# Optimization experiments

Hardware: AMD Instinct MI355X
Metric: run time of the kernel (lower is better)

## Reference

```python
import jax, jax.numpy as jnp
import numpy as np

N_IN = 8192
C_IN, C_H, C_OUT = 64, 32, 32
L = 3
GRID = 64  # parent grid extent (parents live on even coords of a 128^3 grid)


def _build_coords_and_maps():
    """Build sparse voxel coords and the 27-offset kernel map for 3x3x3 stride-1 convs."""
    rng = np.random.RandomState(0)
    pts = rng.randint(0, GRID, size=(4 * N_IN, 3))
    uniq = np.unique(pts, axis=0)
    parents = uniq[rng.permutation(uniq.shape[0])[:N_IN]] * 2  # stride-2 coords in [0,128)
    offs = np.array([[i, j, k] for i in (0, 1) for j in (0, 1) for k in (0, 1)])
    # generative conv transpose kernel=2 stride=2: child k of parent i sits at row i*8+k
    coords = (parents[:, None, :] + offs[None]).reshape(-1, 3)
    n_out = coords.shape[0]
    D = 2 * GRID
    grid = -np.ones((D, D, D), dtype=np.int64)
    grid[coords[:, 0], coords[:, 1], coords[:, 2]] = np.arange(n_out)
    k_offs = np.array([[i, j, k] for i in (-1, 0, 1) for j in (-1, 0, 1) for k in (-1, 0, 1)])
    ins, outs = [], []
    for d in k_offs:
        sh = coords + d
        valid = np.all((sh >= 0) & (sh < D), axis=1)
        j = -np.ones(n_out, dtype=np.int64)
        j[valid] = grid[sh[valid, 0], sh[valid, 1], sh[valid, 2]]
        m = j >= 0
        ins.append(j[m])
        outs.append(np.nonzero(m)[0])
    P = max(len(a) for a in ins)
    nbr_in = np.full((27, P), n_out, dtype=np.int32)   # pad -> dummy zero row
    nbr_out = np.full((27, P), n_out, dtype=np.int32)  # pad -> dummy dropped row
    for k in range(27):
        nbr_in[k, : len(ins[k])] = ins[k]
        nbr_out[k, : len(outs[k])] = outs[k]
    return jnp.asarray(nbr_in), jnp.asarray(nbr_out), n_out


def setup_inputs() -> dict:
    nbr_in, nbr_out, n_out = _build_coords_and_maps()
    key = jax.random.key(0)
    ks = jax.random.split(key, 20)
    w = lambda k, shape, fan: jax.random.normal(k, shape, jnp.float32) / np.float32(np.sqrt(fan))
    C4, C2 = C_OUT // 4, C_OUT // 2
    inp = {
        "x": jax.random.normal(ks[0], (N_IN, C_IN), jnp.float32),
        "W_up": w(ks[1], (8, C_IN, C_H), C_IN),
        "b_up": 0.01 * jax.random.normal(ks[2], (C_H,), jnp.float32),
        "W_conv": w(ks[3], (27, C_H, C_OUT), 27 * C_H),
        "b_conv": 0.01 * jax.random.normal(ks[4], (C_OUT,), jnp.float32),
        "Wb00": w(ks[5], (L, 27, C_OUT, C4), 27 * C_OUT),
        "bb00": 0.01 * jax.random.normal(ks[6], (L, C4), jnp.float32),
        "Wb01": w(ks[7], (L, 27, C4, C2), 27 * C4),
        "bb01": 0.01 * jax.random.normal(ks[8], (L, C2), jnp.float32),
        "Wb10": w(ks[9], (L, C_OUT, C4), C_OUT),
        "bb10": 0.01 * jax.random.normal(ks[10], (L, C4), jnp.float32),
        "Wb11": w(ks[11], (L, 27, C4, C4), 27 * C4),
        "bb11": 0.01 * jax.random.normal(ks[12], (L, C4), jnp.float32),
        "Wb12": w(ks[13], (L, C4, C2), C4),
        "bb12": 0.01 * jax.random.normal(ks[14], (L, C2), jnp.float32),
        "W_cls": w(ks[15], (27, C_OUT, 1), 27 * C_OUT),
        "b_cls": 0.01 * jax.random.normal(ks[16], (1,), jnp.float32),
        "nbr_in": nbr_in,
        "nbr_out": nbr_out,
        # ground-truth occupancy of out coords in target_label (precomputed set membership)
        "target": jax.random.bernoulli(ks[17], 0.5, (n_out,)),
    }
    return inp


def reference(x, W_up, b_up, W_conv, b_conv, Wb00, bb00, Wb01, bb01,
              Wb10, bb10, Wb11, bb11, Wb12, bb12, W_cls, b_cls,
              nbr_in, nbr_out, target):
    n_out = target.shape[0]
    r = jax.nn.relu

    def sconv(f, W, b):
        # 3x3x3 stride-1 sparse conv via shared kernel map: gather -> per-offset GEMM -> scatter-add
        fpad = jnp.concatenate([f, jnp.zeros((1, f.shape[1]), f.dtype)], axis=0)
        g = fpad[nbr_in]                                   # [27, P, Cin]
        contrib = jnp.einsum('kpc,kcd->kpd', g, W)         # [27, P, Cout]
        out = jnp.zeros((n_out + 1, W.shape[2]), f.dtype)
        out = out.at[nbr_out.reshape(-1)].add(contrib.reshape(-1, W.shape[2]))
        return out[:n_out] + b

    # generative transpose kernel=2 stride=2: child k of parent i -> row i*8+k
    up = (jnp.einsum('nc,kcd->nkd', x, W_up) + b_up).reshape(n_out, -1)
    out = r(sconv(r(up), W_conv, b_conv))
    for l in range(L):  # InceptionResNet blocks (PCGCv2-style)
        p0 = sconv(r(sconv(out, Wb00[l], bb00[l])), Wb01[l], bb01[l])
        p1 = r(out @ Wb10[l] + bb10[l])
        p1 = r(sconv(p1, Wb11[l], bb11[l]))
        p1 = p1 @ Wb12[l] + bb12[l]
        out = jnp.concatenate([p0, p1], axis=-1) + out
    out_cls = sconv(out, W_cls, b_cls)                     # [n_out, 1]
    score = out_cls[:, 0]
    keep = score > 0
    # topk(.,1) fallback when everything is negative
    fallback = keep | (jnp.arange(n_out) == jnp.argmax(score))
    keep = jnp.where(jnp.max(score) < 0, fallback, keep)
    # MinkowskiPruning with static shapes: zero-mask pruned rows
    out_pruned = out * keep[:, None].astype(out.dtype)
    return out_pruned, out_cls, target, keep
```

## Files before the change

### kernel.cpp

```cpp
#include <hip/hip_runtime.h>
#include <math.h>

static inline int cdiv(long long a, int b){ return (int)((a + b - 1) / b); }
#define DEVINL __device__ __forceinline__

DEVINL float4 relu4(const float* a){
  return make_float4(fmaxf(a[0],0.f), fmaxf(a[1],0.f), fmaxf(a[2],0.f), fmaxf(a[3],0.f));
}

DEVINL void load32(float* fv, const float* __restrict__ p){
#pragma unroll
  for (int q = 0; q < 8; ++q){
    float4 v = ((const float4*)p)[q];
    fv[4*q]=v.x; fv[4*q+1]=v.y; fv[4*q+2]=v.z; fv[4*q+3]=v.w;
  }
}
DEVINL void load8(float* fv, const float* __restrict__ p){
#pragma unroll
  for (int q = 0; q < 2; ++q){
    float4 v = ((const float4*)p)[q];
    fv[4*q]=v.x; fv[4*q+1]=v.y; fv[4*q+2]=v.z; fv[4*q+3]=v.w;
  }
}

DEVINL int sib_k(int o, int op){
  return 13 + 9*(((op>>2)&1) - ((o>>2)&1))
            + 3*(((op>>1)&1) - ((o>>1)&1))
            +   ((op&1) - (o&1));
}

__global__ void k_rinit(int* __restrict__ cnt, int n){
  int i = blockIdx.x*blockDim.x + threadIdx.x;
  if (i < n) cnt[i] = 0;
}

__global__ void k_rbuild(const int* __restrict__ nin, const int* __restrict__ nout,
                         int* __restrict__ cnt, int* __restrict__ rem, int P, int N){
  int p = blockIdx.x*blockDim.x + threadIdx.x;
  if (p >= 27*P) return;
  int oi = nout[p];
  if (oi >= N) return;
  int j = nin[p];
  if ((oi >> 3) == (j >> 3)) return;
  int k = p / P;
  int pos = atomicAdd(&cnt[oi], 1);
  rem[(size_t)oi*20 + pos] = (j << 5) | k;
}

__global__ __launch_bounds__(256) void k_up(const float* __restrict__ x,
    const float* __restrict__ Wup, const float* __restrict__ bup,
    float* __restrict__ f, int Nn){
  __shared__ float Ws[64*32];
  const int kk = blockIdx.y;
  for (int e = threadIdx.x*4; e < 2048; e += 1024)
    *(float4*)&Ws[e] = *(const float4*)&Wup[(size_t)kk*2048 + e];
  __syncthreads();
  int t = threadIdx.x, cg = t & 7, nr = t >> 3;
  int n = blockIdx.x*32 + nr, c0 = cg*4;
  float4 b4 = *(const float4*)(bup + c0);
  float acc[4] = {b4.x, b4.y, b4.z, b4.w};
  float xr[64];
  const float4* xp = (const float4*)(x + (size_t)n*64);
#pragma unroll
  for (int q = 0; q < 16; ++q){
    float4 v = xp[q];
    xr[4*q]=v.x; xr[4*q+1]=v.y; xr[4*q+2]=v.z; xr[4*q+3]=v.w;
  }
#pragma unroll
  for (int cc = 0; cc < 64; ++cc){
    float4 w = *(const float4*)(Ws + cc*32 + c0);
    acc[0]=fmaf(xr[cc],w.x,acc[0]); acc[1]=fmaf(xr[cc],w.y,acc[1]);
    acc[2]=fmaf(xr[cc],w.z,acc[2]); acc[3]=fmaf(xr[cc],w.w,acc[3]);
  }
  *(float4*)(f + ((size_t)n*8 + kk)*32 + c0) = relu4(acc);
}

__global__ __launch_bounds__(512) void k_conv1(const float* __restrict__ fin,
    const float* __restrict__ Wg, const float* __restrict__ bg,
    const int* __restrict__ cnt, const int* __restrict__ rem,
    float* __restrict__ fout, int N){
  __shared__ float Ws[27*32*8];
  const int cb = blockIdx.y*8;
  int t = threadIdx.x;
  for (int m = t; m < 1728; m += 512){
    int k = m >> 6, r = m & 63, cc = r >> 1, q = r & 1;
    *(float4*)&Ws[k*256 + cc*8 + q*4] =
      *(const float4*)&Wg[((size_t)(k*32 + cc))*32 + cb + q*4];
  }
  __syncthreads();
  int o = t >> 6, lane = t & 63, p = lane >> 1, cg = lane & 1;
  int base = blockIdx.x*256 + p*8;
  int row = base + o, c0 = cg*4;
  float4 b4 = *(const float4*)(bg + cb + c0);
  float acc[4] = {b4.x,b4.y,b4.z,b4.w};
  float fv[32];
#pragma unroll
  for (int op = 0; op < 8; ++op){
    int kk = sib_k(o, op);
    load32(fv, fin + (size_t)(base+op)*32);
    const float* wk = Ws + kk*256 + c0;
#pragma unroll
    for (int cc = 0; cc < 32; ++cc){
      float4 w = *(const float4*)(wk + cc*8);
      acc[0]=fmaf(fv[cc],w.x,acc[0]); acc[1]=fmaf(fv[cc],w.y,acc[1]);
      acc[2]=fmaf(fv[cc],w.z,acc[2]); acc[3]=fmaf(fv[cc],w.w,acc[3]);
    }
  }
  int nrm = cnt[row];
  for (int s = 0; s < nrm; ++s){
    int e = rem[(size_t)row*20 + s];
    int kk = e & 31, j = e >> 5;
    load32(fv, fin + (size_t)j*32);
    const float* wk = Ws + kk*256 + c0;
#pragma unroll
    for (int cc = 0; cc < 32; ++cc){
      float4 w = *(const float4*)(wk + cc*8);
      acc[0]=fmaf(fv[cc],w.x,acc[0]); acc[1]=fmaf(fv[cc],w.y,acc[1]);
      acc[2]=fmaf(fv[cc],w.z,acc[2]); acc[3]=fmaf(fv[cc],w.w,acc[3]);
    }
  }
  *(float4*)(fout + (size_t)row*32 + cb + c0) = relu4(acc);
}

__global__ __launch_bounds__(512) void k_blk_a(const float* __restrict__ fO,
    const float* __restrict__ W00, const float* __restrict__ b00,
    const float* __restrict__ W10, const float* __restrict__ b10,
    const int* __restrict__ cnt, const int* __restrict__ rem,
    float* __restrict__ a8, float* __restrict__ b8, int N){
  __shared__ float Ws[27*256 + 256];
  int t = threadIdx.x;
  for (int m = t; m < 1728; m += 512){
    int k = m >> 6, r = m & 63, cc = r >> 1, q = r & 1;
    *(float4*)&Ws[k*256 + cc*8 + q*4] = ((const float4*)W00)[m];
  }
  if (t < 64) *(float4*)&Ws[6912 + t*4] = ((const float4*)W10)[t];
  __syncthreads();
  int o = t >> 6, lane = t & 63, p = lane >> 1, cg = lane & 1;
  int base = blockIdx.x*256 + p*8;
  int row = base + o, c0 = cg*4;
  float4 b4 = *(const float4*)(b00 + c0);
  float acc[4] = {b4.x,b4.y,b4.z,b4.w};
  float fv[32];
#pragma unroll
  for (int op = 0; op < 8; ++op){
    int kk = sib_k(o, op);
    load32(fv, fO + (size_t)(base+op)*32);
    const float* wk = Ws + kk*256 + c0;
#pragma unroll
    for (int cc = 0; cc < 32; ++cc){
      float4 w = *(const float4*)(wk + cc*8);
      acc[0]=fmaf(fv[cc],w.x,acc[0]); acc[1]=fmaf(fv[cc],w.y,acc[1]);
      acc[2]=fmaf(fv[cc],w.z,acc[2]); acc[3]=fmaf(fv[cc],w.w,acc[3]);
    }
  }
  int nrm = cnt[row];
  for (int s = 0; s < nrm; ++s){
    int e = rem[(size_t)row*20 + s];
    int kk = e & 31, j = e >> 5;
    load32(fv, fO + (size_t)j*32);
    const float* wk = Ws + kk*256 + c0;
#pragma unroll
    for (int cc = 0; cc < 32; ++cc){
      float4 w = *(const float4*)(wk + cc*8);
      acc[0]=fmaf(fv[cc],w.x,acc[0]); acc[1]=fmaf(fv[cc],w.y,acc[1]);
      acc[2]=fmaf(fv[cc],w.z,acc[2]); acc[3]=fmaf(fv[cc],w.w,acc[3]);
    }
  }
  *(float4*)(a8 + (size_t)row*8 + c0) = relu4(acc);
  load32(fv, fO + (size_t)row*32);
  float4 d4 = *(const float4*)(b10 + c0);
  float accb[4] = {d4.x,d4.y,d4.z,d4.w};
#pragma unroll
  for (int cc = 0; cc < 32; ++cc){
    float4 w = *(const float4*)(Ws + 6912 + cc*8 + c0);
    accb[0]=fmaf(fv[cc],w.x,accb[0]); accb[1]=fmaf(fv[cc],w.y,accb[1]);
    accb[2]=fmaf(fv[cc],w.z,accb[2]); accb[3]=fmaf(fv[cc],w.w,accb[3]);
  }
  *(float4*)(b8 + (size_t)row*8 + c0) = relu4(accb);
}

__global__ __launch_bounds__(512) void k_blk_b(const float* __restrict__ a8,
    const float* __restrict__ b8,
    const float* __restrict__ W01, const float* __restrict__ b01,
    const float* __restrict__ W11, const float* __restrict__ b11,
    const float* __restrict__ W12, const float* __restrict__ b12,
    const int* __restrict__ cnt, const int* __restrict__ rem,
    float* __restrict__ fout, int N){
  __shared__ float Ws[27*128 + 27*64 + 128];
  int t = threadIdx.x;
  for (int m = t; m < 864; m += 512)
    ((float4*)Ws)[m] = ((const float4*)W01)[m];
  for (int m = t; m < 432; m += 512)
    ((float4*)(Ws + 3456))[m] = ((const float4*)W11)[m];
  if (t < 32) *(float4*)&Ws[5184 + t*4] = ((const float4*)W12)[t];
  __syncthreads();
  int o = t >> 6, lane = t & 63, p = lane >> 2, cg = lane & 3;
  int base = blockIdx.x*128 + p*8;
  int row = base + o, c0 = cg*4;
  float4 b4 = *(const float4*)(b01 + c0);
  float acc0[4] = {b4.x,b4.y,b4.z,b4.w};
  float t8[8];
#pragma unroll
  for (int c = 0; c < 8; ++c) t8[c] = b11[c];
  float av[8], bv[8];
#pragma unroll
  for (int op = 0; op < 8; ++op){
    int kk = sib_k(o, op);
    load8(av, a8 + (size_t)(base+op)*8);
    load8(bv, b8 + (size_t)(base+op)*8);
    const float* w01k = Ws + kk*128 + c0;
    const float* w11k = Ws + 3456 + kk*64;
#pragma unroll
    for (int cc = 0; cc < 8; ++cc){
      float4 w = *(const float4*)(w01k + cc*16);
      acc0[0]=fmaf(av[cc],w.x,acc0[0]); acc0[1]=fmaf(av[cc],w.y,acc0[1]);
      acc0[2]=fmaf(av[cc],w.z,acc0[2]); acc0[3]=fmaf(av[cc],w.w,acc0[3]);
      float4 u0 = *(const float4*)(w11k + cc*8);
      float4 u1 = *(const float4*)(w11k + cc*8 + 4);
      t8[0]=fmaf(bv[cc],u0.x,t8[0]); t8[1]=fmaf(bv[cc],u0.y,t8[1]);
      t8[2]=fmaf(bv[cc],u0.z,t8[2]); t8[3]=fmaf(bv[cc],u0.w,t8[3]);
      t8[4]=fmaf(bv[cc],u1.x,t8[4]); t8[5]=fmaf(bv[cc],u1.y,t8[5]);
      t8[6]=fmaf(bv[cc],u1.z,t8[6]); t8[7]=fmaf(bv[cc],u1.w,t8[7]);
    }
  }
  int nrm = cnt[row];
  for (int s = 0; s < nrm; ++s){
    int e = rem[(size_t)row*20 + s];
    int kk = e & 31, j = e >> 5;
    load8(av, a8 + (size_t)j*8);
    load8(bv, b8 + (size_t)j*8);
    const float* w01k = Ws + kk*128 + c0;
    const float* w11k = Ws + 3456 + kk*64;
#pragma unroll
    for (int cc = 0; cc < 8; ++cc){
      float4 w = *(const float4*)(w01k + cc*16);
      acc0[0]=fmaf(av[cc],w.x,acc0[0]); acc0[1]=fmaf(av[cc],w.y,acc0[1]);
      acc0[2]=fmaf(av[cc],w.z,acc0[2]); acc0[3]=fmaf(av[cc],w.w,acc0[3]);
      float4 u0 = *(const float4*)(w11k + cc*8);
      float4 u1 = *(const float4*)(w11k + cc*8 + 4);
      t8[0]=fmaf(bv[cc],u0.x,t8[0]); t8[1]=fmaf(bv[cc],u0.y,t8[1]);
      t8[2]=fmaf(bv[cc],u0.z,t8[2]); t8[3]=fmaf(bv[cc],u0.w,t8[3]);
      t8[4]=fmaf(bv[cc],u1.x,t8[4]); t8[5]=fmaf(bv[cc],u1.y,t8[5]);
      t8[6]=fmaf(bv[cc],u1.z,t8[6]); t8[7]=fmaf(bv[cc],u1.w,t8[7]);
    }
  }
#pragma unroll
  for (int c = 0; c < 8; ++c) t8[c] = fmaxf(t8[c], 0.f);
  float4 d4 = *(const float4*)(b12 + c0);
  float acc1[4] = {d4.x,d4.y,d4.z,d4.w};
#pragma unroll
  for (int cc = 0; cc < 8; ++cc){
    float4 w = *(const float4*)(Ws + 5184 + cc*16 + c0);
    acc1[0]=fmaf(t8[cc],w.x,acc1[0]); acc1[1]=fmaf(t8[cc],w.y,acc1[1]);
    acc1[2]=fmaf(t8[cc],w.z,acc1[2]); acc1[3]=fmaf(t8[cc],w.w,acc1[3]);
  }
  float4* o0 = (float4*)(fout + (size_t)row*32 + c0);
  float4* o1 = (float4*)(fout + (size_t)row*32 + 16 + c0);
  float4 v0 = *o0, v1 = *o1;
  v0.x+=acc0[0]; v0.y+=acc0[1]; v0.z+=acc0[2]; v0.w+=acc0[3];
  v1.x+=acc1[0]; v1.y+=acc1[1]; v1.z+=acc1[2]; v1.w+=acc1[3];
  *o0 = v0; *o1 = v1;
}

__global__ __launch_bounds__(256) void k_cls(const float* __restrict__ fO,
    const float* __restrict__ Wc, const float* __restrict__ bc,
    const int* __restrict__ cnt, const int* __restrict__ rem,
    float* __restrict__ cls, int N){
  __shared__ float Ws[27*32];
  int t = threadIdx.x;
  if (t < 216) ((float4*)Ws)[t] = ((const float4*)Wc)[t];
  __syncthreads();
  int o = blockIdx.y*4 + (t >> 6), p = t & 63;
  int base = (blockIdx.x*64 + p)*8;
  int row = base + o;
  float acc = 0.f;
  float fv[32];
#pragma unroll
  for (int op = 0; op < 8; ++op){
    int kk = sib_k(o, op);
    load32(fv, fO + (size_t)(base+op)*32);
    const float* wk = Ws + kk*32;
#pragma unroll
    for (int c4 = 0; c4 < 8; ++c4){
      float4 w = *(const float4*)(wk + c4*4);
      acc = fmaf(fv[4*c4],w.x,acc);   acc = fmaf(fv[4*c4+1],w.y,acc);
      acc = fmaf(fv[4*c4+2],w.z,acc); acc = fmaf(fv[4*c4+3],w.w,acc);
    }
  }
  int nrm = cnt[row];
  for (int s = 0; s < nrm; ++s){
    int e = rem[(size_t)row*20 + s];
    int kk = e & 31, j = e >> 5;
    load32(fv, fO + (size_t)j*32);
    const float* wk = Ws + kk*32;
#pragma unroll
    for (int c4 = 0; c4 < 8; ++c4){
      float4 w = *(const float4*)(wk + c4*4);
      acc = fmaf(fv[4*c4],w.x,acc);   acc = fmaf(fv[4*c4+1],w.y,acc);
      acc = fmaf(fv[4*c4+2],w.z,acc); acc = fmaf(fv[4*c4+3],w.w,acc);
    }
  }
  cls[row] = acc + bc[0];
}

__global__ void k_reduce1(const float* __restrict__ s, float* __restrict__ pmax,
                          int* __restrict__ pidx, int n){
  __shared__ float sm[256]; __shared__ int si[256];
  int t = threadIdx.x;
  float v = -INFINITY; int vi = 0x7fffffff;
  for (int j = blockIdx.x*256 + t; j < n; j += gridDim.x*256){
    float w = s[j];
    if (w > v){ v = w; vi = j; }
  }
  sm[t] = v; si[t] = vi; __syncthreads();
  for (int o = 128; o > 0; o >>= 1){
    if (t < o){
      if (sm[t+o] > sm[t] || (sm[t+o] == sm[t] && si[t+o] < si[t])){ sm[t]=sm[t+o]; si[t]=si[t+o]; }
    }
    __syncthreads();
  }
  if (t == 0){ pmax[blockIdx.x] = sm[0]; pidx[blockIdx.x] = si[0]; }
}

__global__ void k_reduce2(const float* __restrict__ pmax, const int* __restrict__ pidx,
                          float* __restrict__ g, int nb){
  __shared__ float sm[256]; __shared__ int si[256];
  int t = threadIdx.x;
  sm[t] = (t < nb) ? pmax[t] : -INFINITY;
  si[t] = (t < nb) ? pidx[t] : 0x7fffffff;
  __syncthreads();
  for (int o = 128; o > 0; o >>= 1){
    if (t < o){
      if (sm[t+o] > sm[t] || (sm[t+o] == sm[t] && si[t+o] < si[t])){ sm[t]=sm[t+o]; si[t]=si[t+o]; }
    }
    __syncthreads();
  }
  if (t == 0){ g[0] = sm[0]; ((int*)g)[1] = si[0]; }
}

__global__ void k_final(const float* __restrict__ out, const float* __restrict__ cls,
                        const int* __restrict__ target, const float* __restrict__ g,
                        float* __restrict__ dout, int n_out){
  int idx = blockIdx.x*blockDim.x + threadIdx.x;
  if (idx >= n_out*32) return;
  int row = idx >> 5, c = idx & 31;
  float s = cls[row];
  bool keep = s > 0.f;
  if (g[0] < 0.f) keep = keep || (row == ((const int*)g)[1]);
  float km = keep ? 1.f : 0.f;
  dout[idx] = out[idx] * km;
  if (c == 0){
    dout[(size_t)n_out*32 + row] = s;
    dout[(size_t)n_out*33 + row] = (target[row] != 0) ? 1.f : 0.f;
    dout[(size_t)n_out*34 + row] = km;
  }
}

extern "C" void kernel_launch(void* const* d_in, const int* in_sizes, int n_in,
                              void* d_out, int out_size, void* d_ws, size_t ws_size,
                              hipStream_t stream){
  const float* x      = (const float*)d_in[0];
  const float* W_up   = (const float*)d_in[1];
  const float* b_up   = (const float*)d_in[2];
  const float* W_conv = (const float*)d_in[3];
  const float* b_conv = (const float*)d_in[4];
  const float* Wb00   = (const float*)d_in[5];
  const float* bb00   = (const float*)d_in[6];
  const float* Wb01   = (const float*)d_in[7];
  const float* bb01   = (const float*)d_in[8];
  const float* Wb10   = (const float*)d_in[9];
  const float* bb10   = (const float*)d_in[10];
  const float* Wb11   = (const float*)d_in[11];
  const float* bb11   = (const float*)d_in[12];
  const float* Wb12   = (const float*)d_in[13];
  const float* bb12   = (const float*)d_in[14];
  const float* W_cls  = (const float*)d_in[15];
  const float* b_cls  = (const float*)d_in[16];
  const int*   nbr_in = (const int*)d_in[17];
  const int*   nbr_out= (const int*)d_in[18];
  const int*   target = (const int*)d_in[19];

  const int N = in_sizes[19];
  const int P = in_sizes[17] / 27;
  const int pairsT = 27 * P;
  const int Nn = N / 8;

  int*   cnt  = (int*)d_ws;
  int*   rem  = cnt + N;
  float* wsf  = (float*)(rem + (size_t)N*20);
  float* f_tmp = wsf;
  float* f_out = f_tmp + (size_t)N*32;
  float* a8    = f_out + (size_t)N*32;
  float* b8    = a8 + (size_t)N*8;
  float* cls   = b8 + (size_t)N*8;
  float* pmax  = cls + N;
  int*   pidx  = (int*)(pmax + 256);
  float* gm    = pmax + 512;

  const int B = 256;

  k_rinit<<<cdiv(N,B),B,0,stream>>>(cnt, N);
  k_rbuild<<<cdiv((long long)pairsT,B),B,0,stream>>>(nbr_in, nbr_out, cnt, rem, P, N);

  k_up<<<dim3(Nn/32,8),B,0,stream>>>(x, W_up, b_up, f_tmp, Nn);

  k_conv1<<<dim3(N/256,4),512,0,stream>>>(f_tmp, W_conv, b_conv, cnt, rem, f_out, N);

  for (int l = 0; l < 3; ++l){
    k_blk_a<<<N/256,512,0,stream>>>(f_out, Wb00 + (size_t)l*6912, bb00 + l*8,
                                    Wb10 + (size_t)l*256, bb10 + l*8, cnt, rem, a8, b8, N);
    k_blk_b<<<N/128,512,0,stream>>>(a8, b8,
                                    Wb01 + (size_t)l*3456, bb01 + l*16,
                                    Wb11 + (size_t)l*1728, bb11 + l*8,
                                    Wb12 + (size_t)l*128, bb12 + l*16,
                                    cnt, rem, f_out, N);
  }

  k_cls<<<dim3(N/512,2),B,0,stream>>>(f_out, W_cls, b_cls, cnt, rem, cls, N);

  k_reduce1<<<256,256,0,stream>>>(cls, pmax, pidx, N);
  k_reduce2<<<1,256,0,stream>>>(pmax, pidx, gm, 256);

  k_final<<<cdiv((long long)N*32,B),B,0,stream>>>(f_out, cls, target, gm, (float*)d_out, N);
}
```

Measured before the change: 217.7 us.

## Register-block multiple parents per thread in sparse conv kernels to reuse weights

Restructures k_conv1, k_blk_a and k_blk_b so each thread accumulates outputs for several parent voxels (4 or 2) at once. Each shared-memory weight load is then reused across several rows. Channel tiles are widened (16 output channels per block in conv1) and the grid and block shapes are changed to match. The costs are more registers per thread, lower occupancy from bigger weight tiles, and serialized per-row handling of the remaining neighbours.

```diff
diff --git a/kernel.cpp b/kernel.cpp
--- a/kernel.cpp
+++ b/kernel.cpp
@@ -6,21 +6,6 @@
 
 DEVINL float4 relu4(const float* a){
   return make_float4(fmaxf(a[0],0.f), fmaxf(a[1],0.f), fmaxf(a[2],0.f), fmaxf(a[3],0.f));
-}
-
-DEVINL void load32(float* fv, const float* __restrict__ p){
-#pragma unroll
-  for (int q = 0; q < 8; ++q){
-    float4 v = ((const float4*)p)[q];
-    fv[4*q]=v.x; fv[4*q+1]=v.y; fv[4*q+2]=v.z; fv[4*q+3]=v.w;
-  }
-}
-DEVINL void load8(float* fv, const float* __restrict__ p){
-#pragma unroll
-  for (int q = 0; q < 2; ++q){
-    float4 v = ((const float4*)p)[q];
-    fv[4*q]=v.x; fv[4*q+1]=v.y; fv[4*q+2]=v.z; fv[4*q+3]=v.w;
-  }
 }
 
 DEVINL int sib_k(int o, int op){
@@ -79,104 +64,153 @@
     const float* __restrict__ Wg, const float* __restrict__ bg,
     const int* __restrict__ cnt, const int* __restrict__ rem,
     float* __restrict__ fout, int N){
-  __shared__ float Ws[27*32*8];
-  const int cb = blockIdx.y*8;
-  int t = threadIdx.x;
-  for (int m = t; m < 1728; m += 512){
-    int k = m >> 6, r = m & 63, cc = r >> 1, q = r & 1;
-    *(float4*)&Ws[k*256 + cc*8 + q*4] =
-      *(const float4*)&Wg[((size_t)(k*32 + cc))*32 + cb + q*4];
-  }
-  __syncthreads();
-  int o = t >> 6, lane = t & 63, p = lane >> 1, cg = lane & 1;
-  int base = blockIdx.x*256 + p*8;
-  int row = base + o, c0 = cg*4;
-  float4 b4 = *(const float4*)(bg + cb + c0);
-  float acc[4] = {b4.x,b4.y,b4.z,b4.w};
-  float fv[32];
-#pragma unroll
+  __shared__ float Ws[27*512];
+  const int y = blockIdx.y;
+  int t = threadIdx.x;
+  for (int m = t; m < 3456; m += 512){
+    int kk = m >> 7, r = m & 127, cc = r >> 2, c4 = r & 3;
+    *(float4*)&Ws[kk*512 + cc*16 + c4*4] =
+      *(const float4*)&Wg[((size_t)(kk*32+cc))*32 + y*16 + c4*4];
+  }
+  __syncthreads();
+  int o = t >> 6, lane = t & 63;
+  int q = lane >> 2, cg = lane & 3;
+  int pbase = blockIdx.x*64 + q*4;
+  int c0 = cg*4;
+  float4 b4 = *(const float4*)(bg + y*16 + c0);
+  float acc[4][4];
+#pragma unroll
+  for (int i = 0; i < 4; ++i){ acc[i][0]=b4.x; acc[i][1]=b4.y; acc[i][2]=b4.z; acc[i][3]=b4.w; }
+#pragma unroll 1
   for (int op = 0; op < 8; ++op){
     int kk = sib_k(o, op);
-    load32(fv, fin + (size_t)(base+op)*32);
-    const float* wk = Ws + kk*256 + c0;
-#pragma unroll
-    for (int cc = 0; cc < 32; ++cc){
-      float4 w = *(const float4*)(wk + cc*8);
-      acc[0]=fmaf(fv[cc],w.x,acc[0]); acc[1]=fmaf(fv[cc],w.y,acc[1]);
-      acc[2]=fmaf(fv[cc],w.z,acc[2]); acc[3]=fmaf(fv[cc],w.w,acc[3]);
-    }
-  }
-  int nrm = cnt[row];
-  for (int s = 0; s < nrm; ++s){
-    int e = rem[(size_t)row*20 + s];
-    int kk = e & 31, j = e >> 5;
-    load32(fv, fin + (size_t)j*32);
-    const float* wk = Ws + kk*256 + c0;
-#pragma unroll
-    for (int cc = 0; cc < 32; ++cc){
-      float4 w = *(const float4*)(wk + cc*8);
-      acc[0]=fmaf(fv[cc],w.x,acc[0]); acc[1]=fmaf(fv[cc],w.y,acc[1]);
-      acc[2]=fmaf(fv[cc],w.z,acc[2]); acc[3]=fmaf(fv[cc],w.w,acc[3]);
-    }
-  }
-  *(float4*)(fout + (size_t)row*32 + cb + c0) = relu4(acc);
-}
-
-__global__ __launch_bounds__(512) void k_blk_a(const float* __restrict__ fO,
+    const float* wk = Ws + kk*512 + c0;
+    const float* r0 = fin + ((size_t)((pbase+0)*8 + op))*32;
+    const float* r1 = fin + ((size_t)((pbase+1)*8 + op))*32;
+    const float* r2 = fin + ((size_t)((pbase+2)*8 + op))*32;
+    const float* r3 = fin + ((size_t)((pbase+3)*8 + op))*32;
+#pragma unroll
+    for (int h = 0; h < 2; ++h){
+      float fv[4][16];
+#pragma unroll
+      for (int qq = 0; qq < 4; ++qq){
+        float4 v0 = ((const float4*)r0)[h*4+qq];
+        float4 v1 = ((const float4*)r1)[h*4+qq];
+        float4 v2 = ((const float4*)r2)[h*4+qq];
+        float4 v3 = ((const float4*)r3)[h*4+qq];
+        fv[0][4*qq]=v0.x; fv[0][4*qq+1]=v0.y; fv[0][4*qq+2]=v0.z; fv[0][4*qq+3]=v0.w;
+        fv[1][4*qq]=v1.x; fv[1][4*qq+1]=v1.y; fv[1][4*qq+2]=v1.z; fv[1][4*qq+3]=v1.w;
+        fv[2][4*qq]=v2.x; fv[2][4*qq+1]=v2.y; fv[2][4*qq+2]=v2.z; fv[2][4*qq+3]=v2.w;
+        fv[3][4*qq]=v3.x; fv[3][4*qq+1]=v3.y; fv[3][4*qq+2]=v3.z; fv[3][4*qq+3]=v3.w;
+      }
+#pragma unroll
+      for (int cc = 0; cc < 16; ++cc){
+        float4 w = *(const float4*)(wk + (h*16+cc)*16);
+#pragma unroll
+        for (int i = 0; i < 4; ++i){
+          acc[i][0]=fmaf(fv[i][cc],w.x,acc[i][0]);
+          acc[i][1]=fmaf(fv[i][cc],w.y,acc[i][1]);
+          acc[i][2]=fmaf(fv[i][cc],w.z,acc[i][2]);
+          acc[i][3]=fmaf(fv[i][cc],w.w,acc[i][3]);
+        }
+      }
+    }
+  }
+#pragma unroll 1
+  for (int i = 0; i < 4; ++i){
+    int row = (pbase+i)*8 + o;
+    int nrm = cnt[row];
+    for (int s = 0; s < nrm; ++s){
+      int e = rem[(size_t)row*20 + s];
+      int kk = e & 31, jr = e >> 5;
+      const float* fr = fin + (size_t)jr*32;
+      const float* wk = Ws + kk*512 + c0;
+#pragma unroll
+      for (int cc = 0; cc < 32; ++cc){
+        float4 w = *(const float4*)(wk + cc*16);
+        float fx = fr[cc];
+        acc[i][0]=fmaf(fx,w.x,acc[i][0]); acc[i][1]=fmaf(fx,w.y,acc[i][1]);
+        acc[i][2]=fmaf(fx,w.z,acc[i][2]); acc[i][3]=fmaf(fx,w.w,acc[i][3]);
+      }
+    }
+    *(float4*)(fout + (size_t)row*32 + y*16 + c0) = relu4(acc[i]);
+  }
+}
+
+__global__ __launch_bounds__(256) void k_blk_a(const float* __restrict__ fO,
     const float* __restrict__ W00, const float* __restrict__ b00,
     const float* __restrict__ W10, const float* __restrict__ b10,
     const int* __restrict__ cnt, const int* __restrict__ rem,
     float* __restrict__ a8, float* __restrict__ b8, int N){
   __shared__ float Ws[27*256 + 256];
   int t = threadIdx.x;
-  for (int m = t; m < 1728; m += 512){
-    int k = m >> 6, r = m & 63, cc = r >> 1, q = r & 1;
-    *(float4*)&Ws[k*256 + cc*8 + q*4] = ((const float4*)W00)[m];
-  }
+  for (int m = t; m < 1728; m += 256)
+    ((float4*)Ws)[m] = ((const float4*)W00)[m];
   if (t < 64) *(float4*)&Ws[6912 + t*4] = ((const float4*)W10)[t];
   __syncthreads();
-  int o = t >> 6, lane = t & 63, p = lane >> 1, cg = lane & 1;
-  int base = blockIdx.x*256 + p*8;
-  int row = base + o, c0 = cg*4;
+  int w = t >> 6, lane = t & 63;
+  int o = 2*w + (lane >> 5);
+  int h = lane & 31, pp = h >> 1, cg = h & 1;
+  int pbase = blockIdx.x*32 + pp*2;
+  int c0 = cg*4;
   float4 b4 = *(const float4*)(b00 + c0);
-  float acc[4] = {b4.x,b4.y,b4.z,b4.w};
-  float fv[32];
-#pragma unroll
+  float acc[2][4];
+#pragma unroll
+  for (int i = 0; i < 2; ++i){ acc[i][0]=b4.x; acc[i][1]=b4.y; acc[i][2]=b4.z; acc[i][3]=b4.w; }
+#pragma unroll 1
   for (int op = 0; op < 8; ++op){
     int kk = sib_k(o, op);
-    load32(fv, fO + (size_t)(base+op)*32);
     const float* wk = Ws + kk*256 + c0;
+    float fv[2][32];
+#pragma unroll
+    for (int i = 0; i < 2; ++i){
+      const float4* p = (const float4*)(fO + ((size_t)((pbase+i)*8 + op))*32);
+#pragma unroll
+      for (int qq = 0; qq < 8; ++qq){
+        float4 v = p[qq];
+        fv[i][4*qq]=v.x; fv[i][4*qq+1]=v.y; fv[i][4*qq+2]=v.z; fv[i][4*qq+3]=v.w;
+      }
+    }
 #pragma unroll
     for (int cc = 0; cc < 32; ++cc){
-      float4 w = *(const float4*)(wk + cc*8);
-      acc[0]=fmaf(fv[cc],w.x,acc[0]); acc[1]=fmaf(fv[cc],w.y,acc[1]);
-      acc[2]=fmaf(fv[cc],w.z,acc[2]); acc[3]=fmaf(fv[cc],w.w,acc[3]);
-    }
-  }
-  int nrm = cnt[row];
-  for (int s = 0; s < nrm; ++s){
-    int e = rem[(size_t)row*20 + s];
-    int kk = e & 31, j = e >> 5;
-    load32(fv, fO + (size_t)j*32);
-    const float* wk = Ws + kk*256 + c0;
+      float4 wv = *(const float4*)(wk + cc*8);
+#pragma unroll
+      for (int i = 0; i < 2; ++i){
+        acc[i][0]=fmaf(fv[i][cc],wv.x,acc[i][0]); acc[i][1]=fmaf(fv[i][cc],wv.y,acc[i][1]);
+        acc[i][2]=fmaf(fv[i][cc],wv.z,acc[i][2]); acc[i][3]=fmaf(fv[i][cc],wv.w,acc[i][3]);
+      }
+    }
+  }
+#pragma unroll 1
+  for (int i = 0; i < 2; ++i){
+    int row = (pbase+i)*8 + o;
+    int nrm = cnt[row];
+    for (int s = 0; s < nrm; ++s){
+      int e = rem[(size_t)row*20 + s];
+      int kk = e & 31, jr = e >> 5;
+      const float* fr = fO + (size_t)jr*32;
+      const float* wk = Ws + kk*256 + c0;
+#pragma unroll
+      for (int cc = 0; cc < 32; ++cc){
+        float4 wv = *(const float4*)(wk + cc*8);
+        float fx = fr[cc];
+        acc[i][0]=fmaf(fx,wv.x,acc[i][0]); acc[i][1]=fmaf(fx,wv.y,acc[i][1]);
+        acc[i][2]=fmaf(fx,wv.z,acc[i][2]); acc[i][3]=fmaf(fx,wv.w,acc[i][3]);
+      }
+    }
+    *(float4*)(a8 + (size_t)row*8 + c0) = relu4(acc[i]);
+    const float* fr = fO + (size_t)row*32;
+    float4 d4 = *(const float4*)(b10 + c0);
+    float accb[4] = {d4.x,d4.y,d4.z,d4.w};
 #pragma unroll
     for (int cc = 0; cc < 32; ++cc){
-      float4 w = *(const float4*)(wk + cc*8);
-      acc[0]=fmaf(fv[cc],w.x,acc[0]); acc[1]=fmaf(fv[cc],w.y,acc[1]);
-      acc[2]=fmaf(fv[cc],w.z,acc[2]); acc[3]=fmaf(fv[cc],w.w,acc[3]);
-    }
-  }
-  *(float4*)(a8 + (size_t)row*8 + c0) = relu4(acc);
-  load32(fv, fO + (size_t)row*32);
-  float4 d4 = *(const float4*)(b10 + c0);
-  float accb[4] = {d4.x,d4.y,d4.z,d4.w};
-#pragma unroll
-  for (int cc = 0; cc < 32; ++cc){
-    float4 w = *(const float4*)(Ws + 6912 + cc*8 + c0);
-    accb[0]=fmaf(fv[cc],w.x,accb[0]); accb[1]=fmaf(fv[cc],w.y,accb[1]);
-    accb[2]=fmaf(fv[cc],w.z,accb[2]); accb[3]=fmaf(fv[cc],w.w,accb[3]);
-  }
-  *(float4*)(b8 + (size_t)row*8 + c0) = relu4(accb);
+      float4 wv = *(const float4*)(Ws + 6912 + cc*8 + c0);
+      float fx = fr[cc];
+      accb[0]=fmaf(fx,wv.x,accb[0]); accb[1]=fmaf(fx,wv.y,accb[1]);
+      accb[2]=fmaf(fx,wv.z,accb[2]); accb[3]=fmaf(fx,wv.w,accb[3]);
+    }
+    *(float4*)(b8 + (size_t)row*8 + c0) = relu4(accb);
+  }
 }
 
 __global__ __launch_bounds__(512) void k_blk_b(const float* __restrict__ a8,
@@ -194,72 +228,93 @@
     ((float4*)(Ws + 3456))[m] = ((const float4*)W11)[m];
   if (t < 32) *(float4*)&Ws[5184 + t*4] = ((const float4*)W12)[t];
   __syncthreads();
-  int o = t >> 6, lane = t & 63, p = lane >> 2, cg = lane & 3;
-  int base = blockIdx.x*128 + p*8;
-  int row = base + o, c0 = cg*4;
+  int o = t >> 6, lane = t & 63;
+  int q = lane >> 2, cg = lane & 3;
+  int pbase = blockIdx.x*32 + q*2;
+  int c0 = cg*4;
   float4 b4 = *(const float4*)(b01 + c0);
-  float acc0[4] = {b4.x,b4.y,b4.z,b4.w};
-  float t8[8];
-#pragma unroll
-  for (int c = 0; c < 8; ++c) t8[c] = b11[c];
-  float av[8], bv[8];
-#pragma unroll
+  float acc0[2][4];
+  float t8[2][8];
+#pragma unroll
+  for (int i = 0; i < 2; ++i){
+    acc0[i][0]=b4.x; acc0[i][1]=b4.y; acc0[i][2]=b4.z; acc0[i][3]=b4.w;
+#pragma unroll
+    for (int c = 0; c < 8; ++c) t8[i][c] = b11[c];
+  }
+#pragma unroll 1
   for (int op = 0; op < 8; ++op){
     int kk = sib_k(o, op);
-    load8(av, a8 + (size_t)(base+op)*8);
-    load8(bv, b8 + (size_t)(base+op)*8);
     const float* w01k = Ws + kk*128 + c0;
     const float* w11k = Ws + 3456 + kk*64;
+    float av[2][8], bv[2][8];
+#pragma unroll
+    for (int i = 0; i < 2; ++i){
+      const float4* pa = (const float4*)(a8 + ((size_t)((pbase+i)*8 + op))*8);
+      const float4* pb = (const float4*)(b8 + ((size_t)((pbase+i)*8 + op))*8);
+      float4 va0 = pa[0], va1 = pa[1], vb0 = pb[0], vb1 = pb[1];
+      av[i][0]=va0.x; av[i][1]=va0.y; av[i][2]=va0.z; av[i][3]=va0.w;
+      av[i][4]=va1.x; av[i][5]=va1.y; av[i][6]=va1.z; av[i][7]=va1.w;
+      bv[i][0]=vb0.x; bv[i][1]=vb0.y; bv[i][2]=vb0.z; bv[i][3]=vb0.w;
+      bv[i][4]=vb1.x; bv[i][5]=vb1.y; bv[i][6]=vb1.z; bv[i][7]=vb1.w;
+    }
 #pragma unroll
     for (int cc = 0; cc < 8; ++cc){
       float4 w = *(const float4*)(w01k + cc*16);
-      acc0[0]=fmaf(av[cc],w.x,acc0[0]); acc0[1]=fmaf(av[cc],w.y,acc0[1]);
-      acc0[2]=fmaf(av[cc],w.z,acc0[2]); acc0[3]=fmaf(av[cc],w.w,acc0[3]);
       float4 u0 = *(const float4*)(w11k + cc*8);
       float4 u1 = *(const float4*)(w11k + cc*8 + 4);
-      t8[0]=fmaf(bv[cc],u0.x,t8[0]); t8[1]=fmaf(bv[cc],u0.y,t8[1]);
-      t8[2]=fmaf(bv[cc],u0.z,t8[2]); t8[3]=fmaf(bv[cc],u0.w,t8[3]);
-      t8[4]=fmaf(bv[cc],u1.x,t8[4]); t8[5]=fmaf(bv[cc],u1.y,t8[5]);
-      t8[6]=fmaf(bv[cc],u1.z,t8[6]); t8[7]=fmaf(bv[cc],u1.w,t8[7]);
-    }
-  }
-  int nrm = cnt[row];
-  for (int s = 0; s < nrm; ++s){
-    int e = rem[(size_t)row*20 + s];
-    int kk = e & 31, j = e >> 5;
-    load8(av, a8 + (size_t)j*8);
-    load8(bv, b8 + (size_t)j*8);
-    const float* w01k = Ws + kk*128 + c0;
-    const float* w11k = Ws + 3456 + kk*64;
+#pragma unroll
+      for (int i = 0; i < 2; ++i){
+        acc0[i][0]=fmaf(av[i][cc],w.x,acc0[i][0]); acc0[i][1]=fmaf(av[i][cc],w.y,acc0[i][1]);
+        acc0[i][2]=fmaf(av[i][cc],w.z,acc0[i][2]); acc0[i][3]=fmaf(av[i][cc],w.w,acc0[i][3]);
+        t8[i][0]=fmaf(bv[i][cc],u0.x,t8[i][0]); t8[i][1]=fmaf(bv[i][cc],u0.y,t8[i][1]);
+        t8[i][2]=fmaf(bv[i][cc],u0.z,t8[i][2]); t8[i][3]=fmaf(bv[i][cc],u0.w,t8[i][3]);
+        t8[i][4]=fmaf(bv[i][cc],u1.x,t8[i][4]); t8[i][5]=fmaf(bv[i][cc],u1.y,t8[i][5]);
+        t8[i][6]=fmaf(bv[i][cc],u1.z,t8[i][6]); t8[i][7]=fmaf(bv[i][cc],u1.w,t8[i][7]);
+      }
+    }
+  }
+#pragma unroll 1
+  for (int i = 0; i < 2; ++i){
+    int row = (pbase+i)*8 + o;
+    int nrm = cnt[row];
+    for (int s = 0; s < nrm; ++s){
+      int e = rem[(size_t)row*20 + s];
+      int kk = e & 31, jr = e >> 5;
+      const float* fra = a8 + (size_t)jr*8;
+      const float* frb = b8 + (size_t)jr*8;
+      const float* wg0 = Ws + kk*128 + c0;
+      const float* wg1 = Ws + 3456 + kk*64;
+#pragma unroll
+      for (int cc = 0; cc < 8; ++cc){
+        float fa = fra[cc], fb = frb[cc];
+        float4 w = *(const float4*)(wg0 + cc*16);
+        float4 u0 = *(const float4*)(wg1 + cc*8);
+        float4 u1 = *(const float4*)(wg1 + cc*8 + 4);
+        acc0[i][0]=fmaf(fa,w.x,acc0[i][0]); acc0[i][1]=fmaf(fa,w.y,acc0[i][1]);
+        acc0[i][2]=fmaf(fa,w.z,acc0[i][2]); acc0[i][3]=fmaf(fa,w.w,acc0[i][3]);
+        t8[i][0]=fmaf(fb,u0.x,t8[i][0]); t8[i][1]=fmaf(fb,u0.y,t8[i][1]);
+        t8[i][2]=fmaf(fb,u0.z,t8[i][2]); t8[i][3]=fmaf(fb,u0.w,t8[i][3]);
+        t8[i][4]=fmaf(fb,u1.x,t8[i][4]); t8[i][5]=fmaf(fb,u1.y,t8[i][5]);
+        t8[i][6]=fmaf(fb,u1.z,t8[i][6]); t8[i][7]=fmaf(fb,u1.w,t8[i][7]);
+      }
+    }
+#pragma unroll
+    for (int c = 0; c < 8; ++c) t8[i][c] = fmaxf(t8[i][c], 0.f);
+    float4 d4 = *(const float4*)(b12 + c0);
+    float p1[4] = {d4.x,d4.y,d4.z,d4.w};
 #pragma unroll
     for (int cc = 0; cc < 8; ++cc){
-      float4 w = *(const float4*)(w01k + cc*16);
-      acc0[0]=fmaf(av[cc],w.x,acc0[0]); acc0[1]=fmaf(av[cc],w.y,acc0[1]);
-      acc0[2]=fmaf(av[cc],w.z,acc0[2]); acc0[3]=fmaf(av[cc],w.w,acc0[3]);
-      float4 u0 = *(const float4*)(w11k + cc*8);
-      float4 u1 = *(const float4*)(w11k + cc*8 + 4);
-      t8[0]=fmaf(bv[cc],u0.x,t8[0]); t8[1]=fmaf(bv[cc],u0.y,t8[1]);
-      t8[2]=fmaf(bv[cc],u0.z,t8[2]); t8[3]=fmaf(bv[cc],u0.w,t8[3]);
-      t8[4]=fmaf(bv[cc],u1.x,t8[4]); t8[5]=fmaf(bv[cc],u1.y,t8[5]);
-      t8[6]=fmaf(bv[cc],u1.z,t8[6]); t8[7]=fmaf(bv[cc],u1.w,t8[7]);
-    }
-  }
-#pragma unroll
-  for (int c = 0; c < 8; ++c) t8[c] = fmaxf(t8[c], 0.f);
-  float4 d4 = *(const float4*)(b12 + c0);
-  float acc1[4] = {d4.x,d4.y,d4.z,d4.w};
-#pragma unroll
-  for (int cc = 0; cc < 8; ++cc){
-    float4 w = *(const float4*)(Ws + 5184 + cc*16 + c0);
-    acc1[0]=fmaf(t8[cc],w.x,acc1[0]); acc1[1]=fmaf(t8[cc],w.y,acc1[1]);
-    acc1[2]=fmaf(t8[cc],w.z,acc1[2]); acc1[3]=fmaf(t8[cc],w.w,acc1[3]);
-  }
-  float4* o0 = (float4*)(fout + (size_t)row*32 + c0);
-  float4* o1 = (float4*)(fout + (size_t)row*32 + 16 + c0);
-  float4 v0 = *o0, v1 = *o1;
-  v0.x+=acc0[0]; v0.y+=acc0[1]; v0.z+=acc0[2]; v0.w+=acc0[3];
-  v1.x+=acc1[0]; v1.y+=acc1[1]; v1.z+=acc1[2]; v1.w+=acc1[3];
-  *o0 = v0; *o1 = v1;
+      float4 w = *(const float4*)(Ws + 5184 + cc*16 + c0);
+      p1[0]=fmaf(t8[i][cc],w.x,p1[0]); p1[1]=fmaf(t8[i][cc],w.y,p1[1]);
+      p1[2]=fmaf(t8[i][cc],w.z,p1[2]); p1[3]=fmaf(t8[i][cc],w.w,p1[3]);
+    }
+    float4* o0 = (float4*)(fout + (size_t)row*32 + c0);
+    float4* o1 = (float4*)(fout + (size_t)row*32 + 16 + c0);
+    float4 v0 = *o0, v1 = *o1;
+    v0.x+=acc0[i][0]; v0.y+=acc0[i][1]; v0.z+=acc0[i][2]; v0.w+=acc0[i][3];
+    v1.x+=p1[0]; v1.y+=p1[1]; v1.z+=p1[2]; v1.w+=p1[3];
+    *o0 = v0; *o1 = v1;
+  }
 }
 
 __global__ __launch_bounds__(256) void k_cls(const float* __restrict__ fO,
@@ -278,7 +333,12 @@
 #pragma unroll
   for (int op = 0; op < 8; ++op){
     int kk = sib_k(o, op);
-    load32(fv, fO + (size_t)(base+op)*32);
+    const float4* pp = (const float4*)(fO + (size_t)(base+op)*32);
+#pragma unroll
+    for (int qq = 0; qq < 8; ++qq){
+      float4 v = pp[qq];
+      fv[4*qq]=v.x; fv[4*qq+1]=v.y; fv[4*qq+2]=v.z; fv[4*qq+3]=v.w;
+    }
     const float* wk = Ws + kk*32;
 #pragma unroll
     for (int c4 = 0; c4 < 8; ++c4){
@@ -291,7 +351,12 @@
   for (int s = 0; s < nrm; ++s){
     int e = rem[(size_t)row*20 + s];
     int kk = e & 31, j = e >> 5;
-    load32(fv, fO + (size_t)j*32);
+    const float4* pp = (const float4*)(fO + (size_t)j*32);
+#pragma unroll
+    for (int qq = 0; qq < 8; ++qq){
+      float4 v = pp[qq];
+      fv[4*qq]=v.x; fv[4*qq+1]=v.y; fv[4*qq+2]=v.z; fv[4*qq+3]=v.w;
+    }
     const float* wk = Ws + kk*32;
 #pragma unroll
     for (int c4 = 0; c4 < 8; ++c4){
@@ -404,12 +469,12 @@
 
   k_up<<<dim3(Nn/32,8),B,0,stream>>>(x, W_up, b_up, f_tmp, Nn);
 
-  k_conv1<<<dim3(N/256,4),512,0,stream>>>(f_tmp, W_conv, b_conv, cnt, rem, f_out, N);
+  k_conv1<<<dim3(N/512,2),512,0,stream>>>(f_tmp, W_conv, b_conv, cnt, rem, f_out, N);
 
   for (int l = 0; l < 3; ++l){
-    k_blk_a<<<N/256,512,0,stream>>>(f_out, Wb00 + (size_t)l*6912, bb00 + l*8,
+    k_blk_a<<<Nn/32,256,0,stream>>>(f_out, Wb00 + (size_t)l*6912, bb00 + l*8,
                                     Wb10 + (size_t)l*256, bb10 + l*8, cnt, rem, a8, b8, N);
-    k_blk_b<<<N/128,512,0,stream>>>(a8, b8,
+    k_blk_b<<<Nn/32,512,0,stream>>>(a8, b8,
                                     Wb01 + (size_t)l*3456, bb01 + l*16,
                                     Wb11 + (size_t)l*1728, bb11 + l*8,
                                     Wb12 + (size_t)l*128, bb12 + l*16,
```

Result: slower. 666.7 us (+206.2%).

## Register-tile k_up and k_conv1 over four rows to reuse weight loads

Applied to the files above, without the earlier changes.

k_up now loads all eight child weight slices into shared memory once per block, and each thread computes four rows by four channels. k_conv1 moves from 8-channel to 16-channel output slices and also gives each thread four parent rows, so every shared-memory weight read feeds four rows of FMAs. The aim is to cut LDS traffic and redundant weight staging. The cost is more registers per thread, larger shared allocations (64 KB and 54 KB) that may lower occupancy, and fewer blocks in k_conv1.

```diff
diff --git a/kernel.cpp b/kernel.cpp
--- a/kernel.cpp
+++ b/kernel.cpp
@@ -47,79 +47,122 @@
   rem[(size_t)oi*20 + pos] = (j << 5) | k;
 }
 
-__global__ __launch_bounds__(256) void k_up(const float* __restrict__ x,
+__global__ __launch_bounds__(512) void k_up(const float* __restrict__ x,
     const float* __restrict__ Wup, const float* __restrict__ bup,
     float* __restrict__ f, int Nn){
-  __shared__ float Ws[64*32];
-  const int kk = blockIdx.y;
-  for (int e = threadIdx.x*4; e < 2048; e += 1024)
-    *(float4*)&Ws[e] = *(const float4*)&Wup[(size_t)kk*2048 + e];
-  __syncthreads();
-  int t = threadIdx.x, cg = t & 7, nr = t >> 3;
-  int n = blockIdx.x*32 + nr, c0 = cg*4;
+  __shared__ float Ws[8*64*32];
+  int t = threadIdx.x;
+  for (int m = t; m < 4096; m += 512)
+    ((float4*)Ws)[m] = ((const float4*)Wup)[m];
+  __syncthreads();
+  int kk = t >> 6;
+  int lane = t & 63, nq = lane >> 3, cg = lane & 7;
+  int n0 = blockIdx.x*32 + nq*4;
+  int c0 = cg*4;
+  const float* wk = Ws + kk*2048 + c0;
   float4 b4 = *(const float4*)(bup + c0);
-  float acc[4] = {b4.x, b4.y, b4.z, b4.w};
-  float xr[64];
-  const float4* xp = (const float4*)(x + (size_t)n*64);
-#pragma unroll
-  for (int q = 0; q < 16; ++q){
-    float4 v = xp[q];
-    xr[4*q]=v.x; xr[4*q+1]=v.y; xr[4*q+2]=v.z; xr[4*q+3]=v.w;
-  }
-#pragma unroll
-  for (int cc = 0; cc < 64; ++cc){
-    float4 w = *(const float4*)(Ws + cc*32 + c0);
-    acc[0]=fmaf(xr[cc],w.x,acc[0]); acc[1]=fmaf(xr[cc],w.y,acc[1]);
-    acc[2]=fmaf(xr[cc],w.z,acc[2]); acc[3]=fmaf(xr[cc],w.w,acc[3]);
-  }
-  *(float4*)(f + ((size_t)n*8 + kk)*32 + c0) = relu4(acc);
+  float acc[4][4];
+#pragma unroll
+  for (int i = 0; i < 4; ++i){ acc[i][0]=b4.x; acc[i][1]=b4.y; acc[i][2]=b4.z; acc[i][3]=b4.w; }
+#pragma unroll
+  for (int h = 0; h < 8; ++h){
+    float fv[4][8];
+#pragma unroll
+    for (int i = 0; i < 4; ++i){
+      float4 v0 = ((const float4*)(x + (size_t)(n0+i)*64))[h*2+0];
+      float4 v1 = ((const float4*)(x + (size_t)(n0+i)*64))[h*2+1];
+      fv[i][0]=v0.x; fv[i][1]=v0.y; fv[i][2]=v0.z; fv[i][3]=v0.w;
+      fv[i][4]=v1.x; fv[i][5]=v1.y; fv[i][6]=v1.z; fv[i][7]=v1.w;
+    }
+#pragma unroll
+    for (int cc = 0; cc < 8; ++cc){
+      float4 w = *(const float4*)(wk + (h*8+cc)*32);
+#pragma unroll
+      for (int i = 0; i < 4; ++i){
+        acc[i][0]=fmaf(fv[i][cc],w.x,acc[i][0]); acc[i][1]=fmaf(fv[i][cc],w.y,acc[i][1]);
+        acc[i][2]=fmaf(fv[i][cc],w.z,acc[i][2]); acc[i][3]=fmaf(fv[i][cc],w.w,acc[i][3]);
+      }
+    }
+  }
+#pragma unroll
+  for (int i = 0; i < 4; ++i)
+    *(float4*)(f + ((size_t)(n0+i)*8 + kk)*32 + c0) = relu4(acc[i]);
 }
 
 __global__ __launch_bounds__(512) void k_conv1(const float* __restrict__ fin,
     const float* __restrict__ Wg, const float* __restrict__ bg,
     const int* __restrict__ cnt, const int* __restrict__ rem,
     float* __restrict__ fout, int N){
-  __shared__ float Ws[27*32*8];
-  const int cb = blockIdx.y*8;
-  int t = threadIdx.x;
-  for (int m = t; m < 1728; m += 512){
-    int k = m >> 6, r = m & 63, cc = r >> 1, q = r & 1;
-    *(float4*)&Ws[k*256 + cc*8 + q*4] =
-      *(const float4*)&Wg[((size_t)(k*32 + cc))*32 + cb + q*4];
-  }
-  __syncthreads();
-  int o = t >> 6, lane = t & 63, p = lane >> 1, cg = lane & 1;
-  int base = blockIdx.x*256 + p*8;
-  int row = base + o, c0 = cg*4;
-  float4 b4 = *(const float4*)(bg + cb + c0);
-  float acc[4] = {b4.x,b4.y,b4.z,b4.w};
-  float fv[32];
-#pragma unroll
+  __shared__ float Ws[27*512];
+  const int y = blockIdx.y;
+  int t = threadIdx.x;
+  for (int m = t; m < 3456; m += 512){
+    int kk = m >> 7, r = m & 127, cc = r >> 2, c4 = r & 3;
+    *(float4*)&Ws[kk*512 + cc*16 + c4*4] =
+      *(const float4*)&Wg[((size_t)(kk*32+cc))*32 + y*16 + c4*4];
+  }
+  __syncthreads();
+  int o = t >> 6, lane = t & 63;
+  int q = lane >> 2, cg = lane & 3;
+  int pbase = blockIdx.x*64 + q*4;
+  int c0 = cg*4;
+  float4 b4 = *(const float4*)(bg + y*16 + c0);
+  float acc[4][4];
+#pragma unroll
+  for (int i = 0; i < 4; ++i){ acc[i][0]=b4.x; acc[i][1]=b4.y; acc[i][2]=b4.z; acc[i][3]=b4.w; }
+#pragma unroll 1
   for (int op = 0; op < 8; ++op){
     int kk = sib_k(o, op);
-    load32(fv, fin + (size_t)(base+op)*32);
-    const float* wk = Ws + kk*256 + c0;
-#pragma unroll
-    for (int cc = 0; cc < 32; ++cc){
-      float4 w = *(const float4*)(wk + cc*8);
-      acc[0]=fmaf(fv[cc],w.x,acc[0]); acc[1]=fmaf(fv[cc],w.y,acc[1]);
-      acc[2]=fmaf(fv[cc],w.z,acc[2]); acc[3]=fmaf(fv[cc],w.w,acc[3]);
-    }
-  }
-  int nrm = cnt[row];
-  for (int s = 0; s < nrm; ++s){
-    int e = rem[(size_t)row*20 + s];
-    int kk = e & 31, j = e >> 5;
-    load32(fv, fin + (size_t)j*32);
-    const float* wk = Ws + kk*256 + c0;
-#pragma unroll
-    for (int cc = 0; cc < 32; ++cc){
-      float4 w = *(const float4*)(wk + cc*8);
-      acc[0]=fmaf(fv[cc],w.x,acc[0]); acc[1]=fmaf(fv[cc],w.y,acc[1]);
-      acc[2]=fmaf(fv[cc],w.z,acc[2]); acc[3]=fmaf(fv[cc],w.w,acc[3]);
-    }
-  }
-  *(float4*)(fout + (size_t)row*32 + cb + c0) = relu4(acc);
+    const float* wk = Ws + kk*512 + c0;
+#pragma unroll
+    for (int h = 0; h < 4; ++h){
+      float fv[4][8];
+#pragma unroll
+      for (int i = 0; i < 4; ++i){
+        const float4* rp = (const float4*)(fin + ((size_t)((pbase+i)*8 + op))*32);
+        float4 v0 = rp[h*2+0], v1 = rp[h*2+1];
+        fv[i][0]=v0.x; fv[i][1]=v0.y; fv[i][2]=v0.z; fv[i][3]=v0.w;
+        fv[i][4]=v1.x; fv[i][5]=v1.y; fv[i][6]=v1.z; fv[i][7]=v1.w;
+      }
+#pragma unroll
+      for (int cc = 0; cc < 8; ++cc){
+        float4 w = *(const float4*)(wk + (h*8+cc)*16);
+#pragma unroll
+        for (int i = 0; i < 4; ++i){
+          acc[i][0]=fmaf(fv[i][cc],w.x,acc[i][0]); acc[i][1]=fmaf(fv[i][cc],w.y,acc[i][1]);
+          acc[i][2]=fmaf(fv[i][cc],w.z,acc[i][2]); acc[i][3]=fmaf(fv[i][cc],w.w,acc[i][3]);
+        }
+      }
+    }
+  }
+#pragma unroll 1
+  for (int i = 0; i < 4; ++i){
+    int row = (pbase+i)*8 + o;
+    int nrm = cnt[row];
+    for (int s = 0; s < nrm; ++s){
+      int e = rem[(size_t)row*20 + s];
+      int kk = e & 31, jr = e >> 5;
+      const float* wk = Ws + kk*512 + c0;
+      const float4* fr = (const float4*)(fin + (size_t)jr*32);
+#pragma unroll
+      for (int qq = 0; qq < 8; ++qq){
+        float4 v = fr[qq];
+        float4 w0 = *(const float4*)(wk + (qq*4+0)*16);
+        float4 w1 = *(const float4*)(wk + (qq*4+1)*16);
+        float4 w2 = *(const float4*)(wk + (qq*4+2)*16);
+        float4 w3 = *(const float4*)(wk + (qq*4+3)*16);
+        acc[i][0]=fmaf(v.x,w0.x,acc[i][0]); acc[i][1]=fmaf(v.x,w0.y,acc[i][1]);
+        acc[i][2]=fmaf(v.x,w0.z,acc[i][2]); acc[i][3]=fmaf(v.x,w0.w,acc[i][3]);
+        acc[i][0]=fmaf(v.y,w1.x,acc[i][0]); acc[i][1]=fmaf(v.y,w1.y,acc[i][1]);
+        acc[i][2]=fmaf(v.y,w1.z,acc[i][2]); acc[i][3]=fmaf(v.y,w1.w,acc[i][3]);
+        acc[i][0]=fmaf(v.z,w2.x,acc[i][0]); acc[i][1]=fmaf(v.z,w2.y,acc[i][1]);
+        acc[i][2]=fmaf(v.z,w2.z,acc[i][2]); acc[i][3]=fmaf(v.z,w2.w,acc[i][3]);
+        acc[i][0]=fmaf(v.w,w3.x,acc[i][0]); acc[i][1]=fmaf(v.w,w3.y,acc[i][1]);
+        acc[i][2]=fmaf(v.w,w3.z,acc[i][2]); acc[i][3]=fmaf(v.w,w3.w,acc[i][3]);
+      }
+    }
+    *(float4*)(fout + (size_t)row*32 + y*16 + c0) = relu4(acc[i]);
+  }
 }
 
 __global__ __launch_bounds__(512) void k_blk_a(const float* __restrict__ fO,
@@ -402,9 +445,9 @@
   k_rinit<<<cdiv(N,B),B,0,stream>>>(cnt, N);
   k_rbuild<<<cdiv((long long)pairsT,B),B,0,stream>>>(nbr_in, nbr_out, cnt, rem, P, N);
 
-  k_up<<<dim3(Nn/32,8),B,0,stream>>>(x, W_up, b_up, f_tmp, Nn);
-
-  k_conv1<<<dim3(N/256,4),512,0,stream>>>(f_tmp, W_conv, b_conv, cnt, rem, f_out, N);
+  k_up<<<Nn/32,512,0,stream>>>(x, W_up, b_up, f_tmp, Nn);
+
+  k_conv1<<<dim3(N/512,2),512,0,stream>>>(f_tmp, W_conv, b_conv, cnt, rem, f_out, N);
 
   for (int l = 0; l < 3; ++l){
     k_blk_a<<<N/256,512,0,stream>>>(f_out, Wb00 + (size_t)l*6912, bb00 + l*8,
```

New measurement: 254.8 us. 17.0% more time.
